# Kernel optimization log

Hardware: AMD Instinct MI355X
Metric: run time of the kernel (lower is better)

The kernel has to match this reference:

```python
import jax, jax.numpy as jnp
import numpy as np

B, N, D = 4, 2048, 256
H = 8
HD = D // H
FF = 1024
EPS = 1e-5


def layer_norm(x, g, b):
    mu = jnp.mean(x, axis=-1, keepdims=True)
    var = jnp.mean((x - mu) ** 2, axis=-1, keepdims=True)
    return (x - mu) * jax.lax.rsqrt(var + EPS) * g + b


def setup_inputs() -> dict:
    key = jax.random.key(0)
    ks = jax.random.split(key, 12)
    s = 0.02
    return {
        "tokens": jax.random.normal(ks[0], (B, N, D), dtype=jnp.float32),
        "key_padding_mask": jnp.zeros((B, N), dtype=bool),
        "ln1_g": jnp.ones((D,), jnp.float32),
        "ln1_b": jnp.zeros((D,), jnp.float32),
        "wq": jax.random.normal(ks[1], (D, D), jnp.float32) * s,
        "bq": jnp.zeros((D,), jnp.float32),
        "wk": jax.random.normal(ks[2], (D, D), jnp.float32) * s,
        "bk": jnp.zeros((D,), jnp.float32),
        "wv": jax.random.normal(ks[3], (D, D), jnp.float32) * s,
        "bv": jnp.zeros((D,), jnp.float32),
        "wo": jax.random.normal(ks[4], (D, D), jnp.float32) * s,
        "bo": jnp.zeros((D,), jnp.float32),
        "ln2_g": jnp.ones((D,), jnp.float32),
        "ln2_b": jnp.zeros((D,), jnp.float32),
        "w1": jax.random.normal(ks[5], (D, FF), jnp.float32) * s,
        "b1": jnp.zeros((FF,), jnp.float32),
        "w2": jax.random.normal(ks[6], (FF, D), jnp.float32) * s,
        "b2": jnp.zeros((D,), jnp.float32),
    }


def reference(tokens, key_padding_mask, ln1_g, ln1_b, wq, bq, wk, bk, wv, bv,
              wo, bo, ln2_g, ln2_b, w1, b1, w2, b2):
    x = tokens
    # --- self-attention sublayer (pre-LN) ---
    xn = layer_norm(x, ln1_g, ln1_b)
    q = (xn @ wq + bq).reshape(B, N, H, HD).transpose(0, 2, 1, 3)  # [B,H,N,HD]
    k = (xn @ wk + bk).reshape(B, N, H, HD).transpose(0, 2, 1, 3)
    v = (xn @ wv + bv).reshape(B, N, H, HD).transpose(0, 2, 1, 3)
    scores = jnp.einsum('bhqd,bhkd->bhqk', q, k) / np.sqrt(HD).astype(np.float32)
    scores = jnp.where(key_padding_mask[:, None, None, :], -jnp.inf, scores)
    probs = jax.nn.softmax(scores, axis=-1)
    attn = jnp.einsum('bhqk,bhkd->bhqd', probs, v)
    attn = attn.transpose(0, 2, 1, 3).reshape(B, N, D)
    x = x + (attn @ wo + bo)
    # --- feed-forward sublayer (pre-LN) ---
    xn2 = layer_norm(x, ln2_g, ln2_b)
    h = jax.nn.gelu(xn2 @ w1 + b1, approximate=False)  # torch GELU is exact erf
    x = x + (h @ w2 + b2)
    return x
```

## Files before the change

### kernel.cpp

```cpp
#include <hip/hip_runtime.h>
#include <cmath>

typedef __attribute__((ext_vector_type(8))) __bf16 bf16x8;
typedef __attribute__((ext_vector_type(4))) __bf16 bf16x4;
typedef __attribute__((ext_vector_type(4))) float  f32x4;

constexpr int NB   = 4;
constexpr int SEQ  = 2048;
constexpr int DM   = 256;
constexpr int NH   = 8;
constexpr int DH   = 32;
constexpr int DFF  = 1024;
constexpr int MTOK = NB * SEQ;

__global__ __launch_bounds__(256) void ln_kernel(const float* __restrict__ x,
                                                 const float* __restrict__ g,
                                                 const float* __restrict__ b,
                                                 __bf16* __restrict__ out) {
  int wave = threadIdx.x >> 6, lane = threadIdx.x & 63;
  int row = blockIdx.x * 4 + wave;
  const float* xr = x + (size_t)row * DM;
  f32x4 v = *(const f32x4*)(xr + lane * 4);
  float s  = v[0] + v[1] + v[2] + v[3];
  float sq = v[0]*v[0] + v[1]*v[1] + v[2]*v[2] + v[3]*v[3];
  #pragma unroll
  for (int off = 1; off < 64; off <<= 1) {
    s  += __shfl_xor(s, off);
    sq += __shfl_xor(sq, off);
  }
  float mu  = s * (1.0f / DM);
  float var = sq * (1.0f / DM) - mu * mu;
  float rs  = rsqrtf(var + 1e-5f);
  f32x4 gv = *(const f32x4*)(g + lane * 4);
  f32x4 bv = *(const f32x4*)(b + lane * 4);
  bf16x4 o;
  #pragma unroll
  for (int i = 0; i < 4; ++i) o[i] = (__bf16)((v[i] - mu) * rs * gv[i] + bv[i]);
  *(bf16x4*)(out + (size_t)row * DM + lane * 4) = o;
}

__global__ __launch_bounds__(256) void prep_kernel(
    const float* __restrict__ wq, const float* __restrict__ wk, const float* __restrict__ wv,
    const float* __restrict__ wo, const float* __restrict__ w1, const float* __restrict__ w2,
    const unsigned char* __restrict__ mask, const float* __restrict__ tokens,
    const float* __restrict__ ln1g, const float* __restrict__ ln1b,
    __bf16* __restrict__ wqkvT, __bf16* __restrict__ woT,
    __bf16* __restrict__ w1T, __bf16* __restrict__ w2T,
    float* __restrict__ madd_g, __bf16* __restrict__ xn1) {
  __shared__ float tile[32][33];
  int z = blockIdx.z;
  int tid = threadIdx.x;
  if (z == 6) {
    if (blockIdx.x) return;
    int idx = blockIdx.y * 256 + tid;
    madd_g[idx] = mask[idx] ? -__builtin_inff() : 0.0f;
    return;
  }
  if (z >= 7) {
    int lb = blockIdx.y * 32 + blockIdx.x;
    int row = (z - 7) * 4096 + lb * 4 + (tid >> 6);
    int lane = tid & 63;
    const float* xr = tokens + (size_t)row * DM;
    f32x4 v = *(const f32x4*)(xr + lane * 4);
    float s  = v[0] + v[1] + v[2] + v[3];
    float sq = v[0]*v[0] + v[1]*v[1] + v[2]*v[2] + v[3]*v[3];
    #pragma unroll
    for (int off = 1; off < 64; off <<= 1) {
      s  += __shfl_xor(s, off);
      sq += __shfl_xor(sq, off);
    }
    float mu  = s * (1.0f / DM);
    float var = sq * (1.0f / DM) - mu * mu;
    float rs  = rsqrtf(var + 1e-5f);
    f32x4 gv = *(const f32x4*)(ln1g + lane * 4);
    f32x4 bv = *(const f32x4*)(ln1b + lane * 4);
    bf16x4 o;
    #pragma unroll
    for (int i = 0; i < 4; ++i) o[i] = (__bf16)((v[i] - mu) * rs * gv[i] + bv[i]);
    *(bf16x4*)(xn1 + (size_t)row * DM + lane * 4) = o;
    return;
  }
  const float* W; __bf16* Wt; int K, N;
  if      (z == 0) { W = wq; Wt = wqkvT;          K = 256;  N = 256;  }
  else if (z == 1) { W = wk; Wt = wqkvT + 65536;  K = 256;  N = 256;  }
  else if (z == 2) { W = wv; Wt = wqkvT + 131072; K = 256;  N = 256;  }
  else if (z == 3) { W = wo; Wt = woT;            K = 256;  N = 256;  }
  else if (z == 4) { W = w1; Wt = w1T;            K = 256;  N = 1024; }
  else             { W = w2; Wt = w2T;            K = 1024; N = 256;  }
  int n0 = blockIdx.x * 32, k0 = blockIdx.y * 32;
  if (n0 >= N || k0 >= K) return;
  {
    int kl = tid >> 3, n4 = (tid & 7) * 4;
    f32x4 v = *(const f32x4*)(W + (size_t)(k0 + kl) * N + n0 + n4);
    tile[kl][n4 + 0] = v[0]; tile[kl][n4 + 1] = v[1];
    tile[kl][n4 + 2] = v[2]; tile[kl][n4 + 3] = v[3];
  }
  __syncthreads();
  {
    int nl = tid >> 3, k4 = (tid & 7) * 4;
    bf16x4 o;
    #pragma unroll
    for (int i = 0; i < 4; ++i) o[i] = (__bf16)tile[k4 + i][nl];
    *(bf16x4*)(Wt + (size_t)(n0 + nl) * K + k0 + k4) = o;
  }
}

__global__ __launch_bounds__(256) void transpose_v(const __bf16* __restrict__ V,
                                                   __bf16* __restrict__ Vt) {
  __shared__ __bf16 tile[64][40];
  int tok0 = blockIdx.x * 64;
  int bh = blockIdx.y;
  int tid = threadIdx.x;
  {
    int tl = tid >> 2, h8 = (tid & 3) * 8;
    *(bf16x8*)&tile[tl][h8] = *(const bf16x8*)(V + ((size_t)bh * SEQ + tok0 + tl) * DH + h8);
  }
  __syncthreads();
  {
    int hl = tid >> 3, t8 = (tid & 7) * 8;
    bf16x8 o;
    #pragma unroll
    for (int i = 0; i < 8; ++i) o[i] = tile[t8 + i][hl];
    *(bf16x8*)(Vt + ((size_t)bh * DH + hl) * SEQ + tok0 + t8) = o;
  }
}

template<int BM, int BN, int EP>
__global__ __launch_bounds__(256) void gemm_bt(
    const __bf16* __restrict__ A, const __bf16* __restrict__ Bt,
    int M, int N, int K,
    const float* __restrict__ bias,
    const float* __restrict__ bq, const float* __restrict__ bk, const float* __restrict__ bv,
    const float* __restrict__ resid, float* __restrict__ outf,
    __bf16* __restrict__ outb,
    __bf16* __restrict__ outq, __bf16* __restrict__ outk, __bf16* __restrict__ outv) {
  constexpr int MT = BM / 32, NT = BN / 32;
  __shared__ __bf16 As[BM][72];
  __shared__ __bf16 Bs[BN][72];
  int tid = threadIdx.x;
  int wave = tid >> 6, lane = tid & 63;
  int wm = wave >> 1, wn = wave & 1;
  int quad = lane >> 4, l16 = lane & 15;
  int m0 = blockIdx.x * BM, n0 = blockIdx.y * BN;

  f32x4 acc[MT][NT];
  #pragma unroll
  for (int mt = 0; mt < MT; ++mt)
    #pragma unroll
    for (int nt = 0; nt < NT; ++nt)
      #pragma unroll
      for (int r = 0; r < 4; ++r) acc[mt][nt][r] = 0.0f;

  for (int kt = 0; kt < K; kt += 64) {
    __syncthreads();
    #pragma unroll
    for (int p = 0; p < BM / 32; ++p) {
      int idx = p * 256 + tid, row = idx >> 3, c8 = (idx & 7) * 8;
      *(bf16x8*)&As[row][c8] = *(const bf16x8*)(A + (size_t)(m0 + row) * K + kt + c8);
    }
    #pragma unroll
    for (int p = 0; p < BN / 32; ++p) {
      int idx = p * 256 + tid, row = idx >> 3, c8 = (idx & 7) * 8;
      *(bf16x8*)&Bs[row][c8] = *(const bf16x8*)(Bt + (size_t)(n0 + row) * K + kt + c8);
    }
    __syncthreads();
    #pragma unroll
    for (int ks = 0; ks < 2; ++ks) {
      bf16x8 af[MT], bfr[NT];
      #pragma unroll
      for (int mt = 0; mt < MT; ++mt)
        af[mt] = *(const bf16x8*)&As[wm * (BM / 2) + mt * 16 + l16][ks * 32 + quad * 8];
      #pragma unroll
      for (int nt = 0; nt < NT; ++nt)
        bfr[nt] = *(const bf16x8*)&Bs[wn * (BN / 2) + nt * 16 + l16][ks * 32 + quad * 8];
      #pragma unroll
      for (int mt = 0; mt < MT; ++mt)
        #pragma unroll
        for (int nt = 0; nt < NT; ++nt)
          acc[mt][nt] = __builtin_amdgcn_mfma_f32_16x16x32_bf16(af[mt], bfr[nt], acc[mt][nt], 0, 0, 0);
    }
  }

  #pragma unroll
  for (int mt = 0; mt < MT; ++mt)
  #pragma unroll
  for (int nt = 0; nt < NT; ++nt)
  #pragma unroll
  for (int r = 0; r < 4; ++r) {
    int gm = m0 + wm * (BM / 2) + mt * 16 + quad * 4 + r;
    int gn = n0 + wn * (BN / 2) + nt * 16 + l16;
    float v = acc[mt][nt][r];
    if constexpr (EP == 0) {
      int which = gn >> 8, nn = gn & 255;
      const float* bp = which == 0 ? bq : (which == 1 ? bk : bv);
      v += bp[nn];
      int h = nn >> 5, hd = nn & 31;
      int bb = gm >> 11, tok = gm & 2047;
      __bf16* dst = which == 0 ? outq : (which == 1 ? outk : outv);
      dst[(((size_t)(bb * NH + h)) * SEQ + tok) * DH + hd] = (__bf16)v;
    } else if constexpr (EP == 1) {
      v += bias[gn] + resid[(size_t)gm * N + gn];
      outf[(size_t)gm * N + gn] = v;
    } else {
      v += bias[gn];
      outb[(size_t)gm * N + gn] = (__bf16)(0.5f * v * (1.0f + erff(v * 0.70710678118654752f)));
    }
  }
}

__global__ __launch_bounds__(256) void attn_kernel(
    const __bf16* __restrict__ Q, const __bf16* __restrict__ K,
    const __bf16* __restrict__ Vt, const float* __restrict__ madd_g,
    __bf16* __restrict__ out) {
  constexpr float C2 = 0.2550350030061664f;
  __shared__ __bf16 Ks[128][40];
  __shared__ __bf16 Vs[32][136];
  __shared__ __bf16 Ps[4][16][136];
  int bh = blockIdx.x;
  int q0 = blockIdx.y * 64;
  int b  = bh >> 3, h = bh & 7;
  int tid = threadIdx.x;
  int wave = tid >> 6, lane = tid & 63;
  int quad = lane >> 4, l16 = lane & 15;
  const __bf16* Qb = Q  + (size_t)bh * SEQ * DH;
  const __bf16* Kb = K  + (size_t)bh * SEQ * DH;
  const __bf16* Vb = Vt + (size_t)bh * DH * SEQ;
  const float* maddb = madd_g + b * SEQ;
  int qw = q0 + wave * 16;

  bf16x8 qf = *(const bf16x8*)(Qb + (size_t)(qw + l16) * DH + quad * 8);

  bf16x8 ones;
  #pragma unroll
  for (int i = 0; i < 8; ++i) ones[i] = (__bf16)1.0f;

  f32x4 o[2], ol;
  #pragma unroll
  for (int nt = 0; nt < 2; ++nt)
    #pragma unroll
    for (int r = 0; r < 4; ++r) o[nt][r] = 0.0f;
  #pragma unroll
  for (int r = 0; r < 4; ++r) ol[r] = 0.0f;

  for (int kt = 0; kt < SEQ / 128; ++kt) {
    int k0 = kt * 128;
    __syncthreads();
    #pragma unroll
    for (int p = 0; p < 2; ++p) {
      int idx = p * 256 + tid, row = idx >> 2, c8 = (idx & 3) * 8;
      *(bf16x8*)&Ks[row][c8] = *(const bf16x8*)(Kb + (size_t)(k0 + row) * DH + c8);
    }
    #pragma unroll
    for (int p = 0; p < 2; ++p) {
      int idx = p * 256 + tid, row = idx >> 4, c8 = (idx & 15) * 8;
      *(bf16x8*)&Vs[row][c8] = *(const bf16x8*)(Vb + (size_t)row * SEQ + k0 + c8);
    }
    __syncthreads();

    f32x4 s[8];
    f32x4 zf; zf[0] = zf[1] = zf[2] = zf[3] = 0.0f;
    #pragma unroll
    for (int mt = 0; mt < 8; ++mt) {
      bf16x8 kf = *(const bf16x8*)&Ks[mt * 16 + l16][quad * 8];
      s[mt] = __builtin_amdgcn_mfma_f32_16x16x32_bf16(kf, qf, zf, 0, 0, 0);
    }

    #pragma unroll
    for (int mt = 0; mt < 8; ++mt) {
      f32x4 md = *(const f32x4*)(maddb + k0 + mt * 16 + quad * 4);
      bf16x4 pv;
      #pragma unroll
      for (int r = 0; r < 4; ++r)
        pv[r] = (__bf16)__builtin_amdgcn_exp2f(fmaf(s[mt][r], C2, md[r]));
      *(bf16x4*)&Ps[wave][l16][mt * 16 + quad * 4] = pv;
    }

    #pragma unroll
    for (int ks = 0; ks < 4; ++ks) {
      bf16x8 pf = *(const bf16x8*)&Ps[wave][l16][ks * 32 + quad * 8];
      #pragma unroll
      for (int nt = 0; nt < 2; ++nt) {
        bf16x8 vf = *(const bf16x8*)&Vs[nt * 16 + l16][ks * 32 + quad * 8];
        o[nt] = __builtin_amdgcn_mfma_f32_16x16x32_bf16(pf, vf, o[nt], 0, 0, 0);
      }
      ol = __builtin_amdgcn_mfma_f32_16x16x32_bf16(pf, ones, ol, 0, 0, 0);
    }
  }

  #pragma unroll
  for (int r = 0; r < 4; ++r) ol[r] = 1.0f / ol[r];
  #pragma unroll
  for (int nt = 0; nt < 2; ++nt)
  #pragma unroll
  for (int r = 0; r < 4; ++r) {
    int q   = qw + quad * 4 + r;
    int col = h * DH + nt * 16 + l16;
    out[((size_t)(b * SEQ + q)) * DM + col] = (__bf16)(o[nt][r] * ol[r]);
  }
}

extern "C" void kernel_launch(void* const* d_in, const int* in_sizes, int n_in,
                              void* d_out, int out_size, void* d_ws, size_t ws_size,
                              hipStream_t stream) {
  const float* tokens = (const float*)d_in[0];
  const unsigned char* mask = (const unsigned char*)d_in[1];
  const float* ln1g = (const float*)d_in[2];
  const float* ln1b = (const float*)d_in[3];
  const float* wq = (const float*)d_in[4];
  const float* bq = (const float*)d_in[5];
  const float* wk = (const float*)d_in[6];
  const float* bk = (const float*)d_in[7];
  const float* wv = (const float*)d_in[8];
  const float* bv = (const float*)d_in[9];
  const float* wo = (const float*)d_in[10];
  const float* bo = (const float*)d_in[11];
  const float* ln2g = (const float*)d_in[12];
  const float* ln2b = (const float*)d_in[13];
  const float* w1 = (const float*)d_in[14];
  const float* b1 = (const float*)d_in[15];
  const float* w2 = (const float*)d_in[16];
  const float* b2 = (const float*)d_in[17];
  float* out = (float*)d_out;
  char* ws = (char*)d_ws;

  __bf16* wqkvT = (__bf16*)(ws + 0);
  __bf16* woT   = (__bf16*)(ws + 393216);
  __bf16* w1T   = (__bf16*)(ws + 524288);
  __bf16* w2T   = (__bf16*)(ws + 1048576);
  __bf16* xn1   = (__bf16*)(ws + 1572864);
  __bf16* qb    = (__bf16*)(ws + 5767168);
  __bf16* kb    = (__bf16*)(ws + 9961472);
  __bf16* vb    = (__bf16*)(ws + 14155776);
  __bf16* vt    = (__bf16*)(ws + 18350080);
  __bf16* attn  = (__bf16*)(ws + 22544384);
  float*  x1    = (float*)(ws + 26738688);
  __bf16* xn2   = (__bf16*)(ws + 35127296);
  __bf16* hbuf  = (__bf16*)(ws + 39321600);
  float*  madd  = (float*)(ws + 56098816);

  prep_kernel<<<dim3(32, 32, 9), 256, 0, stream>>>(
      wq, wk, wv, wo, w1, w2, mask, tokens, ln1g, ln1b,
      wqkvT, woT, w1T, w2T, madd, xn1);

  gemm_bt<128, 128, 0><<<dim3(64, 6), 256, 0, stream>>>(
      xn1, wqkvT, MTOK, 768, 256, nullptr, bq, bk, bv,
      nullptr, nullptr, nullptr, qb, kb, vb);

  transpose_v<<<dim3(SEQ / 64, 32), 256, 0, stream>>>(vb, vt);

  attn_kernel<<<dim3(32, SEQ / 64), 256, 0, stream>>>(qb, kb, vt, madd, attn);

  gemm_bt<128, 64, 1><<<dim3(64, 4), 256, 0, stream>>>(
      attn, woT, MTOK, 256, 256, bo, nullptr, nullptr, nullptr,
      tokens, x1, nullptr, nullptr, nullptr, nullptr);

  ln_kernel<<<MTOK / 4, 256, 0, stream>>>(x1, ln2g, ln2b, xn2);

  gemm_bt<128, 128, 2><<<dim3(64, 8), 256, 0, stream>>>(
      xn2, w1T, MTOK, DFF, 256, b1, nullptr, nullptr, nullptr,
      nullptr, nullptr, hbuf, nullptr, nullptr, nullptr);

  gemm_bt<128, 64, 1><<<dim3(64, 4), 256, 0, stream>>>(
      hbuf, w2T, MTOK, 256, DFF, b2, nullptr, nullptr, nullptr,
      x1, out, nullptr, nullptr, nullptr, nullptr);
}
```

Measured before the change: 214.6 us.

## Use direct global-to-LDS loads with XOR swizzle in GEMM; drop LDS staging in attention

The GEMM tile loads now go straight from global memory into LDS through global_load_lds, which skips the register round trip. To keep fragment reads free of bank conflicts without the old padding, the LDS layout uses an XOR-swizzled column group. The attention kernel drops its shared K/V staging and the two barriers per tile, so each wave reads K and V fragments directly from global memory (relying on the cache). This removes synchronisation and LDS traffic, but every wave now refetches K/V from global memory and the V reads are strided.

```diff
diff --git a/kernel.cpp b/kernel.cpp
--- a/kernel.cpp
+++ b/kernel.cpp
@@ -4,6 +4,9 @@
 typedef __attribute__((ext_vector_type(8))) __bf16 bf16x8;
 typedef __attribute__((ext_vector_type(4))) __bf16 bf16x4;
 typedef __attribute__((ext_vector_type(4))) float  f32x4;
+
+typedef __attribute__((address_space(3))) char       lds_c;
+typedef __attribute__((address_space(1))) const char glob_c;
 
 constexpr int NB   = 4;
 constexpr int SEQ  = 2048;
@@ -135,13 +138,15 @@
     __bf16* __restrict__ outb,
     __bf16* __restrict__ outq, __bf16* __restrict__ outk, __bf16* __restrict__ outv) {
   constexpr int MT = BM / 32, NT = BN / 32;
-  __shared__ __bf16 As[BM][72];
-  __shared__ __bf16 Bs[BN][72];
+  __shared__ __bf16 As[BM * 64];
+  __shared__ __bf16 Bs[BN * 64];
   int tid = threadIdx.x;
   int wave = tid >> 6, lane = tid & 63;
   int wm = wave >> 1, wn = wave & 1;
   int quad = lane >> 4, l16 = lane & 15;
   int m0 = blockIdx.x * BM, n0 = blockIdx.y * BN;
+  int lrow = lane >> 3;
+  int lcg  = ((lane & 7) ^ lrow) * 8;
 
   f32x4 acc[MT][NT];
   #pragma unroll
@@ -154,25 +159,33 @@
   for (int kt = 0; kt < K; kt += 64) {
     __syncthreads();
     #pragma unroll
-    for (int p = 0; p < BM / 32; ++p) {
-      int idx = p * 256 + tid, row = idx >> 3, c8 = (idx & 7) * 8;
-      *(bf16x8*)&As[row][c8] = *(const bf16x8*)(A + (size_t)(m0 + row) * K + kt + c8);
-    }
-    #pragma unroll
-    for (int p = 0; p < BN / 32; ++p) {
-      int idx = p * 256 + tid, row = idx >> 3, c8 = (idx & 7) * 8;
-      *(bf16x8*)&Bs[row][c8] = *(const bf16x8*)(Bt + (size_t)(n0 + row) * K + kt + c8);
+    for (int i = 0; i < BM / 32; ++i) {
+      int rbase = wave * (BM / 4) + i * 8;
+      __builtin_amdgcn_global_load_lds(
+          (glob_c*)(A + (size_t)(m0 + rbase + lrow) * K + kt + lcg),
+          (lds_c*)&As[rbase * 64], 16, 0, 0);
+    }
+    #pragma unroll
+    for (int i = 0; i < BN / 32; ++i) {
+      int rbase = wave * (BN / 4) + i * 8;
+      __builtin_amdgcn_global_load_lds(
+          (glob_c*)(Bt + (size_t)(n0 + rbase + lrow) * K + kt + lcg),
+          (lds_c*)&Bs[rbase * 64], 16, 0, 0);
     }
     __syncthreads();
     #pragma unroll
     for (int ks = 0; ks < 2; ++ks) {
       bf16x8 af[MT], bfr[NT];
       #pragma unroll
-      for (int mt = 0; mt < MT; ++mt)
-        af[mt] = *(const bf16x8*)&As[wm * (BM / 2) + mt * 16 + l16][ks * 32 + quad * 8];
-      #pragma unroll
-      for (int nt = 0; nt < NT; ++nt)
-        bfr[nt] = *(const bf16x8*)&Bs[wn * (BN / 2) + nt * 16 + l16][ks * 32 + quad * 8];
+      for (int mt = 0; mt < MT; ++mt) {
+        int row = wm * (BM / 2) + mt * 16 + l16;
+        af[mt] = *(const bf16x8*)&As[row * 64 + (((ks * 4 + quad) ^ (l16 & 7)) * 8)];
+      }
+      #pragma unroll
+      for (int nt = 0; nt < NT; ++nt) {
+        int row = wn * (BN / 2) + nt * 16 + l16;
+        bfr[nt] = *(const bf16x8*)&Bs[row * 64 + (((ks * 4 + quad) ^ (l16 & 7)) * 8)];
+      }
       #pragma unroll
       for (int mt = 0; mt < MT; ++mt)
         #pragma unroll
@@ -213,8 +226,6 @@
     const __bf16* __restrict__ Vt, const float* __restrict__ madd_g,
     __bf16* __restrict__ out) {
   constexpr float C2 = 0.2550350030061664f;
-  __shared__ __bf16 Ks[128][40];
-  __shared__ __bf16 Vs[32][136];
   __shared__ __bf16 Ps[4][16][136];
   int bh = blockIdx.x;
   int q0 = blockIdx.y * 64;
@@ -244,24 +255,12 @@
 
   for (int kt = 0; kt < SEQ / 128; ++kt) {
     int k0 = kt * 128;
-    __syncthreads();
-    #pragma unroll
-    for (int p = 0; p < 2; ++p) {
-      int idx = p * 256 + tid, row = idx >> 2, c8 = (idx & 3) * 8;
-      *(bf16x8*)&Ks[row][c8] = *(const bf16x8*)(Kb + (size_t)(k0 + row) * DH + c8);
-    }
-    #pragma unroll
-    for (int p = 0; p < 2; ++p) {
-      int idx = p * 256 + tid, row = idx >> 4, c8 = (idx & 15) * 8;
-      *(bf16x8*)&Vs[row][c8] = *(const bf16x8*)(Vb + (size_t)row * SEQ + k0 + c8);
-    }
-    __syncthreads();
 
     f32x4 s[8];
     f32x4 zf; zf[0] = zf[1] = zf[2] = zf[3] = 0.0f;
     #pragma unroll
     for (int mt = 0; mt < 8; ++mt) {
-      bf16x8 kf = *(const bf16x8*)&Ks[mt * 16 + l16][quad * 8];
+      bf16x8 kf = *(const bf16x8*)(Kb + (size_t)(k0 + mt * 16 + l16) * DH + quad * 8);
       s[mt] = __builtin_amdgcn_mfma_f32_16x16x32_bf16(kf, qf, zf, 0, 0, 0);
     }
 
@@ -280,7 +279,7 @@
       bf16x8 pf = *(const bf16x8*)&Ps[wave][l16][ks * 32 + quad * 8];
       #pragma unroll
       for (int nt = 0; nt < 2; ++nt) {
-        bf16x8 vf = *(const bf16x8*)&Vs[nt * 16 + l16][ks * 32 + quad * 8];
+        bf16x8 vf = *(const bf16x8*)(Vb + (size_t)(nt * 16 + l16) * SEQ + k0 + ks * 32 + quad * 8);
         o[nt] = __builtin_amdgcn_mfma_f32_16x16x32_bf16(pf, vf, o[nt], 0, 0, 0);
       }
       ol = __builtin_amdgcn_mfma_f32_16x16x32_bf16(pf, ones, ol, 0, 0, 0);
```

Measured after the change: 252.0 us. 17.5% more time.
